# Performance work log

Measured on AMD Instinct MI355X. Metric: run time of the kernel, lower is better.

The kernel has to match this reference:

```python
import jax, jax.numpy as jnp
import numpy as np

N_CLIN = 38
N_PIX = 36
N_NODES = N_CLIN + N_PIX  # 74
FV = 128
B = 1024
HID = 512
N_OUT = 1


def _base_edges():
    # Faithful to Network.get_edges: self-edges for all nodes, then for each
    # pixel node i, bidirectional edges to every clinical node.
    ids = np.arange(N_NODES)
    parts = [np.stack([ids, ids])]
    c = np.arange(N_CLIN)
    for i in range(N_CLIN, N_NODES):
        ii = np.full(N_CLIN, i)
        parts.append(np.stack([ii, c]))
        parts.append(np.stack([c, ii]))
    return np.concatenate(parts, axis=1)  # (2, 2810)


def setup_inputs() -> dict:
    key = jax.random.key(0)
    ks = jax.random.split(key, 10)
    base = _base_edges()  # (2, E0)
    # Batched edge index: per-sample copy offset by ind*N_NODES (batch-major order,
    # matching the torch.cat loop).
    offs = np.arange(B)[None, :, None] * N_NODES  # (1, B, 1)
    edge_index = (base[:, None, :] + offs).reshape(2, -1)  # (2, B*E0)
    s = 1.0 / np.sqrt(FV)
    return {
        "clinical_embeddings": jax.random.normal(ks[0], (B, N_CLIN, FV), jnp.float32),
        "image_embeddings": jax.random.normal(ks[1], (B, N_PIX, FV), jnp.float32),
        # RMRM graph-net params (single message-passing layer, fv_dim -> fv_dim)
        "W_self": jax.random.normal(ks[2], (FV, FV), jnp.float32) * s,
        "W_msg": jax.random.normal(ks[3], (FV, FV), jnp.float32) * s,
        "b_g": jnp.zeros((FV,), jnp.float32),
        # OutputBlock MLP params: fv_dim*(n_clinical+1)=4992 -> 512 -> 1
        "W1": jax.random.normal(ks[4], (FV * (N_CLIN + 1), HID), jnp.float32) * (1.0 / np.sqrt(FV * (N_CLIN + 1))),
        "b1": jnp.zeros((HID,), jnp.float32),
        "W2": jax.random.normal(ks[5], (HID, N_OUT), jnp.float32) * (1.0 / np.sqrt(HID)),
        "b2": jnp.zeros((N_OUT,), jnp.float32),
        "edge_index": jnp.asarray(edge_index, jnp.int32),
    }


def reference(clinical_embeddings, image_embeddings, W_self, W_msg, b_g, W1, b1, W2, b2, edge_index):
    # Assemble node features: [B, n_nodes, fv] -> flat [B*n_nodes, fv]
    x = jnp.concatenate([clinical_embeddings, image_embeddings], axis=1)
    x = x.reshape(-1, FV)
    src, dst = edge_index[0], edge_index[1]
    n_total = B * N_NODES
    # Mean-aggregated message passing (RMRM layer): gather + segment-sum
    msg = jax.ops.segment_sum(x[src], dst, num_segments=n_total)  # [B*N, FV]
    deg = jax.ops.segment_sum(jnp.ones_like(src, jnp.float32), dst, num_segments=n_total)
    agg = msg / deg[:, None]
    h = jax.nn.relu(x @ W_self + agg @ W_msg + b_g)  # [B*N, FV]
    h = h.reshape(B, N_NODES, FV)
    graph_fvs_c = h[:, :N_CLIN]          # [B, 38, FV]
    graph_fvs_i = h[:, N_CLIN:]          # [B, 36, FV]
    # AvgPool2d(6,6) over [B, FV, 6, 6] == mean over the 36 pixel nodes
    gap = graph_fvs_i.mean(axis=1)       # [B, FV]
    combined = jnp.concatenate([graph_fvs_c, gap[:, None, :]], axis=1).reshape(B, -1)
    # OutputBlock MLP
    out = jax.nn.relu(combined @ W1 + b1) @ W2 + b2  # [B, 1]
    return out
```

## Files before the change

### kernel.cpp

```cpp
#include <hip/hip_runtime.h>

#define FV 128
#define NCLIN 38
#define NPIX 36
#define NTOT 74
#define BATCH 1024
#define HID 512
#define COMB 4992
#define XPAD 136

typedef __attribute__((ext_vector_type(4))) float f32x4;
typedef __attribute__((ext_vector_type(8))) short s16x8;

#define WS_WCT  0
#define WS_WIT  8192
#define WS_WMT  16384
#define WS_COMB 24576
#define WS_W1T  2580480

__device__ __forceinline__ unsigned short bf16_rne(float f) {
    union { float f; unsigned int u; } v; v.f = f;
    unsigned int u = v.u;
    u += 0x7fffu + ((u >> 16) & 1u);
    return (unsigned short)(u >> 16);
}
__device__ __forceinline__ float bf2f(unsigned short h) {
    union { unsigned int u; float f; } v; v.u = ((unsigned int)h) << 16;
    return v.f;
}

__global__ __launch_bounds__(256) void k_prep(
    const float* __restrict__ wself, const float* __restrict__ wmsg,
    const float* __restrict__ b2, float* __restrict__ ws,
    float* __restrict__ out)
{
    const int t = threadIdx.x;
    if (blockIdx.x == 8) {
        const float v = b2[0];
#pragma unroll
        for (int j = 0; j < 4; ++j) out[t + j * 256] = v;
        return;
    }
    unsigned short* WcT = (unsigned short*)(ws + WS_WCT);
    unsigned short* WiT = (unsigned short*)(ws + WS_WIT);
    unsigned short* WmT = (unsigned short*)(ws + WS_WMT);
    const int r  = blockIdx.x * 16 + (t >> 4);
    const int f0 = (t & 15) * 8;
#pragma unroll
    for (int j = 0; j < 8; ++j) {
        const int f = f0 + j;
        const int idx = r * 128 + f;
        const float wm = wmsg[idx];
        const float s  = wself[idx];
        WcT[f * 128 + r] = bf16_rne(s + wm * (1.0f / 37.0f));
        WiT[f * 128 + r] = bf16_rne(s + wm * (1.0f / 39.0f));
        WmT[f * 128 + r] = bf16_rne(wm);
    }
}

union __align__(16) SmemMain {
    float tile[64][65];
    struct {
        unsigned short xl[NTOT * XPAD];
        unsigned short sab[2 * 128];
        float tcv[128];
        float tiv[128];
    } b;
};

__global__ __launch_bounds__(256) void k_main(
    const float* __restrict__ clin, const float* __restrict__ img,
    const float* __restrict__ bg, const float* __restrict__ W1,
    float* __restrict__ ws)
{
    const int blk = blockIdx.x;
    const int t   = threadIdx.x;
    __shared__ SmemMain sm;

    if (blk >= BATCH) {
        const int u  = blk - BATCH;
        unsigned short* W1T = (unsigned short*)(ws + WS_W1T);
        const int k0 = (u >> 3) * 64;
        const int n0 = (u & 7) * 64;
        const int r16 = t >> 4;
        const int c4  = (t & 15) * 4;
#pragma unroll
        for (int p = 0; p < 4; ++p) {
            const int r = p * 16 + r16;
            const float4 v = *(const float4*)&W1[(size_t)(k0 + r) * HID + n0 + c4];
            sm.tile[r][c4 + 0] = v.x; sm.tile[r][c4 + 1] = v.y;
            sm.tile[r][c4 + 2] = v.z; sm.tile[r][c4 + 3] = v.w;
        }
        __syncthreads();
        const int j  = t >> 2;
        const int i0 = (t & 3) * 16;
        unsigned short tmp[16];
#pragma unroll
        for (int s = 0; s < 16; ++s) tmp[s] = bf16_rne(sm.tile[i0 + s][j]);
        unsigned short* dst = &W1T[(size_t)(n0 + j) * COMB + k0 + i0];
        *(uint4*)&dst[0] = *(uint4*)&tmp[0];
        *(uint4*)&dst[8] = *(uint4*)&tmp[8];
        return;
    }

    const unsigned short* WcT = (const unsigned short*)(ws + WS_WCT);
    const unsigned short* WiT = (const unsigned short*)(ws + WS_WIT);
    const unsigned short* WmT = (const unsigned short*)(ws + WS_WMT);
    const int wave = t >> 6;
    const int lane = t & 63;
    const int l16  = lane & 15;
    const int q    = lane >> 4;
    const int n0   = wave * 32 + l16;
    const int b    = blk;

    const float* xc = clin + (size_t)b * NCLIN * FV;
    const float* xi = img  + (size_t)b * NPIX * FV;
    for (int i = t; i < NCLIN * 32; i += 256) {
        const int row = i >> 5, c4 = (i & 31) * 4;
        const float4 v = *(const float4*)&xc[row * 128 + c4];
        ushort4 u;
        u.x = bf16_rne(v.x); u.y = bf16_rne(v.y);
        u.z = bf16_rne(v.z); u.w = bf16_rne(v.w);
        *(ushort4*)&sm.b.xl[row * XPAD + c4] = u;
    }
    for (int i = t; i < NPIX * 32; i += 256) {
        const int row = i >> 5, c4 = (i & 31) * 4;
        const float4 v = *(const float4*)&xi[row * 128 + c4];
        ushort4 u;
        u.x = bf16_rne(v.x); u.y = bf16_rne(v.y);
        u.z = bf16_rne(v.z); u.w = bf16_rne(v.w);
        *(ushort4*)&sm.b.xl[(NCLIN + row) * XPAD + c4] = u;
    }
    __syncthreads();

    const int f = t & 127;
    if (t < 128) {
        float s = 0.f;
#pragma unroll
        for (int n = 0; n < NCLIN; ++n) s += bf2f(sm.b.xl[n * XPAD + f]);
        sm.b.sab[128 + f] = bf16_rne(s * (1.0f / 39.0f));
    } else {
        float s = 0.f;
#pragma unroll
        for (int n = 0; n < NPIX; ++n) s += bf2f(sm.b.xl[(NCLIN + n) * XPAD + f]);
        sm.b.sab[f] = bf16_rne(s * (1.0f / 37.0f));
    }
    __syncthreads();

    {
        const int am = (l16 < 2) ? l16 : 0;
        f32x4 ta = {}, tb = {};
#pragma unroll
        for (int kk = 0; kk < 4; ++kk) {
            const int ko = kk * 32 + q * 8;
            const s16x8 av  = *(const s16x8*)&sm.b.sab[am * 128 + ko];
            const s16x8 bv0 = *(const s16x8*)&WmT[(n0)      * 128 + ko];
            const s16x8 bv1 = *(const s16x8*)&WmT[(n0 + 16) * 128 + ko];
            ta = __builtin_amdgcn_mfma_f32_16x16x32_bf16(av, bv0, ta, 0, 0, 0);
            tb = __builtin_amdgcn_mfma_f32_16x16x32_bf16(av, bv1, tb, 0, 0, 0);
        }
        if (q == 0) {
            const int c0 = wave * 32 + l16;
            const int c1 = c0 + 16;
            const float bg0 = bg[c0], bg1 = bg[c1];
            sm.b.tcv[c0] = ta[0] + bg0;  sm.b.tiv[c0] = ta[1] + bg0;
            sm.b.tcv[c1] = tb[0] + bg1;  sm.b.tiv[c1] = tb[1] + bg1;
        }
    }
    __syncthreads();

    unsigned short* combined =
        (unsigned short*)(ws + WS_COMB) + (size_t)b * COMB;

#pragma unroll
    for (int phase = 0; phase < 2; ++phase) {
        const int NN   = phase ? NPIX : NCLIN;
        const int xoff = phase ? NCLIN : 0;
        const unsigned short* WT = phase ? WiT : WcT;
        const float* tvv = phase ? sm.b.tiv : sm.b.tcv;

        const int r0 = xoff + ((l16      < NN) ? l16      : (NN - 1));
        const int r1 = xoff + ((16 + l16 < NN) ? 16 + l16 : (NN - 1));
        const int r2 = xoff + ((32 + l16 < NN) ? 32 + l16 : (NN - 1));

        f32x4 acc[3][2] = {};
#pragma unroll
        for (int kk = 0; kk < 4; ++kk) {
            const int ko = kk * 32 + q * 8;
            const s16x8 a0 = *(const s16x8*)&sm.b.xl[r0 * XPAD + ko];
            const s16x8 a1 = *(const s16x8*)&sm.b.xl[r1 * XPAD + ko];
            const s16x8 a2 = *(const s16x8*)&sm.b.xl[r2 * XPAD + ko];
            const s16x8 b0 = *(const s16x8*)&WT[(n0)      * 128 + ko];
            const s16x8 b1v = *(const s16x8*)&WT[(n0 + 16) * 128 + ko];
            acc[0][0] = __builtin_amdgcn_mfma_f32_16x16x32_bf16(a0, b0,  acc[0][0], 0, 0, 0);
            acc[0][1] = __builtin_amdgcn_mfma_f32_16x16x32_bf16(a0, b1v, acc[0][1], 0, 0, 0);
            acc[1][0] = __builtin_amdgcn_mfma_f32_16x16x32_bf16(a1, b0,  acc[1][0], 0, 0, 0);
            acc[1][1] = __builtin_amdgcn_mfma_f32_16x16x32_bf16(a1, b1v, acc[1][1], 0, 0, 0);
            acc[2][0] = __builtin_amdgcn_mfma_f32_16x16x32_bf16(a2, b0,  acc[2][0], 0, 0, 0);
            acc[2][1] = __builtin_amdgcn_mfma_f32_16x16x32_bf16(a2, b1v, acc[2][1], 0, 0, 0);
        }

        const float t0 = tvv[wave * 32 + l16];
        const float t1 = tvv[wave * 32 + 16 + l16];

        if (phase == 0) {
#pragma unroll
            for (int rt = 0; rt < 3; ++rt) {
#pragma unroll
                for (int r = 0; r < 4; ++r) {
                    const int node = rt * 16 + q * 4 + r;
                    if (node < NCLIN) {
                        combined[node * 128 + wave * 32 + l16] =
                            bf16_rne(fmaxf(acc[rt][0][r] + t0, 0.f));
                        combined[node * 128 + wave * 32 + 16 + l16] =
                            bf16_rne(fmaxf(acc[rt][1][r] + t1, 0.f));
                    }
                }
            }
        } else {
            float g0 = 0.f, g1 = 0.f;
#pragma unroll
            for (int rt = 0; rt < 3; ++rt) {
#pragma unroll
                for (int r = 0; r < 4; ++r) {
                    const int node = rt * 16 + q * 4 + r;
                    if (node < NPIX) {
                        g0 += fmaxf(acc[rt][0][r] + t0, 0.f);
                        g1 += fmaxf(acc[rt][1][r] + t1, 0.f);
                    }
                }
            }
            g0 += __shfl_xor(g0, 16); g0 += __shfl_xor(g0, 32);
            g1 += __shfl_xor(g1, 16); g1 += __shfl_xor(g1, 32);
            if (q == 0) {
                combined[NCLIN * 128 + wave * 32 + l16] =
                    bf16_rne(g0 * (1.0f / 36.0f));
                combined[NCLIN * 128 + wave * 32 + 16 + l16] =
                    bf16_rne(g1 * (1.0f / 36.0f));
            }
        }
    }
}

__global__ __launch_bounds__(256) void k_gemm_out(
    const float* __restrict__ b1, const float* __restrict__ W2,
    float* __restrict__ ws, float* __restrict__ out)
{
    const unsigned short* Abase = (const unsigned short*)(ws + WS_COMB);
    const unsigned short* Bbase = (const unsigned short*)(ws + WS_W1T);
    const int m0 = (blockIdx.x & 15) * 64;
    const int n0 = (blockIdx.x >> 4) * 64;

    __shared__ __align__(16) unsigned short As[2][64 * 64];
    __shared__ __align__(16) unsigned short Bs[2][64 * 64];

    const int t    = threadIdx.x;
    const int wave = t >> 6;
    const int lane = t & 63;
    const int wm   = (wave & 1) * 32;
    const int wn   = (wave >> 1) * 32;
    const int l16  = lane & 15;
    const int q    = lane >> 4;

    const int srow = t >> 2;
    const int c0   = (t & 3) * 2;
    const unsigned short* gA = Abase + (size_t)(m0 + srow) * COMB + c0 * 8;
    const unsigned short* gB = Bbase + (size_t)(n0 + srow) * COMB + c0 * 8;
    const int sw0 = srow * 64 + ((c0     + srow) & 7) * 8;
    const int sw1 = srow * 64 + ((c0 + 1 + srow) & 7) * 8;

    int aoff[2][2], boff[2][2];
#pragma unroll
    for (int i = 0; i < 2; ++i) {
#pragma unroll
        for (int kk = 0; kk < 2; ++kk) {
            const int rot = (kk * 4 + q + l16) & 7;
            aoff[i][kk] = (wm + 16 * i + l16) * 64 + rot * 8;
            boff[i][kk] = (wn + 16 * i + l16) * 64 + rot * 8;
        }
    }

    f32x4 acc[2][2] = {};

    *(uint4*)&As[0][sw0] = *(const uint4*)(gA);
    *(uint4*)&As[0][sw1] = *(const uint4*)(gA + 8);
    *(uint4*)&Bs[0][sw0] = *(const uint4*)(gB);
    *(uint4*)&Bs[0][sw1] = *(const uint4*)(gB + 8);

    int cur = 0;
    for (int it = 0; it < 78; ++it) {
        __syncthreads();
        if (it + 1 < 78) {
            const int kk  = (it + 1) * 64;
            const int nxt = cur ^ 1;
            *(uint4*)&As[nxt][sw0] = *(const uint4*)(gA + kk);
            *(uint4*)&As[nxt][sw1] = *(const uint4*)(gA + kk + 8);
            *(uint4*)&Bs[nxt][sw0] = *(const uint4*)(gB + kk);
            *(uint4*)&Bs[nxt][sw1] = *(const uint4*)(gB + kk + 8);
        }

#pragma unroll
        for (int kk = 0; kk < 2; ++kk) {
            const s16x8 a0 = *(const s16x8*)&As[cur][aoff[0][kk]];
            const s16x8 a1 = *(const s16x8*)&As[cur][aoff[1][kk]];
            const s16x8 b0 = *(const s16x8*)&Bs[cur][boff[0][kk]];
            const s16x8 b1v = *(const s16x8*)&Bs[cur][boff[1][kk]];
            acc[0][0] = __builtin_amdgcn_mfma_f32_16x16x32_bf16(a0, b0,  acc[0][0], 0, 0, 0);
            acc[0][1] = __builtin_amdgcn_mfma_f32_16x16x32_bf16(a0, b1v, acc[0][1], 0, 0, 0);
            acc[1][0] = __builtin_amdgcn_mfma_f32_16x16x32_bf16(a1, b0,  acc[1][0], 0, 0, 0);
            acc[1][1] = __builtin_amdgcn_mfma_f32_16x16x32_bf16(a1, b1v, acc[1][1], 0, 0, 0);
        }
        cur ^= 1;
    }

    const int colA = n0 + wn + l16;
    const int colB = colA + 16;
    const float b1a = b1[colA], b1b = b1[colB];
    const float w2a = W2[colA], w2b = W2[colB];

#pragma unroll
    for (int i = 0; i < 2; ++i) {
#pragma unroll
        for (int r = 0; r < 4; ++r) {
            const int mr = m0 + wm + 16 * i + q * 4 + r;
            float v = fmaxf(acc[i][0][r] + b1a, 0.f) * w2a
                    + fmaxf(acc[i][1][r] + b1b, 0.f) * w2b;
            v += __shfl_xor(v, 1);
            v += __shfl_xor(v, 2);
            v += __shfl_xor(v, 4);
            v += __shfl_xor(v, 8);
            if (l16 == 0) atomicAdd(&out[mr], v);
        }
    }
}

extern "C" void kernel_launch(void* const* d_in, const int* in_sizes, int n_in,
                              void* d_out, int out_size, void* d_ws, size_t ws_size,
                              hipStream_t stream) {
    const float* clin  = (const float*)d_in[0];
    const float* img   = (const float*)d_in[1];
    const float* wself = (const float*)d_in[2];
    const float* wmsg  = (const float*)d_in[3];
    const float* bg    = (const float*)d_in[4];
    const float* W1    = (const float*)d_in[5];
    const float* b1    = (const float*)d_in[6];
    const float* W2    = (const float*)d_in[7];
    const float* b2    = (const float*)d_in[8];
    float* ws  = (float*)d_ws;
    float* out = (float*)d_out;

    k_prep<<<dim3(9), 256, 0, stream>>>(wself, wmsg, b2, ws, out);
    k_main<<<dim3(BATCH + 624), 256, 0, stream>>>(clin, img, bg, W1, ws);
    k_gemm_out<<<dim3(128), 256, 0, stream>>>(b1, W2, ws, out);
}
```

Before: 175.4 us.

## Split-K the output GEMM into partial buffers with a separate reduction epilogue

The 1024x512x4992 output GEMM is split along K into 8 slices, with 64x128 tiles on a 16x4x8 grid (512 blocks instead of 128). Each slice writes fp32 partial sums to workspace. A new k_out kernel sums the partials, applies bias, ReLU and the W2 dot product, and writes the output directly, so the atomics and the b2 pre-initialisation are no longer needed. Global loads are now register-prefetched two stages ahead to overlap with MFMA. The cost is about 16 MB of extra partial-sum traffic and one more kernel launch.

```diff
diff --git a/kernel.cpp b/kernel.cpp
--- a/kernel.cpp
+++ b/kernel.cpp
@@ -17,6 +17,8 @@
 #define WS_WMT  16384
 #define WS_COMB 24576
 #define WS_W1T  2580480
+#define WS_Z    3858432
+#define ZSTRIDE (BATCH * HID)
 
 __device__ __forceinline__ unsigned short bf16_rne(float f) {
     union { float f; unsigned int u; } v; v.f = f;
@@ -31,16 +33,9 @@
 
 __global__ __launch_bounds__(256) void k_prep(
     const float* __restrict__ wself, const float* __restrict__ wmsg,
-    const float* __restrict__ b2, float* __restrict__ ws,
-    float* __restrict__ out)
+    float* __restrict__ ws)
 {
     const int t = threadIdx.x;
-    if (blockIdx.x == 8) {
-        const float v = b2[0];
-#pragma unroll
-        for (int j = 0; j < 4; ++j) out[t + j * 256] = v;
-        return;
-    }
     unsigned short* WcT = (unsigned short*)(ws + WS_WCT);
     unsigned short* WiT = (unsigned short*)(ws + WS_WIT);
     unsigned short* WmT = (unsigned short*)(ws + WS_WMT);
@@ -242,61 +237,87 @@
     }
 }
 
-__global__ __launch_bounds__(256) void k_gemm_out(
-    const float* __restrict__ b1, const float* __restrict__ W2,
-    float* __restrict__ ws, float* __restrict__ out)
+__global__ __launch_bounds__(256) void k_gemm_mfma(float* __restrict__ ws)
 {
     const unsigned short* Abase = (const unsigned short*)(ws + WS_COMB);
     const unsigned short* Bbase = (const unsigned short*)(ws + WS_W1T);
-    const int m0 = (blockIdx.x & 15) * 64;
-    const int n0 = (blockIdx.x >> 4) * 64;
+    const int m0    = blockIdx.x * 64;
+    const int n0    = blockIdx.y * 128;
+    const int ks    = blockIdx.z;
+    const int kbase = (ks < 6) ? 640 * ks : 3840 + 576 * (ks - 6);
+    const int kit   = (ks < 6) ? 10 : 9;
+    float* Z = ws + WS_Z + (size_t)ks * ZSTRIDE;
 
     __shared__ __align__(16) unsigned short As[2][64 * 64];
-    __shared__ __align__(16) unsigned short Bs[2][64 * 64];
+    __shared__ __align__(16) unsigned short Bs[2][128 * 64];
 
     const int t    = threadIdx.x;
     const int wave = t >> 6;
     const int lane = t & 63;
     const int wm   = (wave & 1) * 32;
-    const int wn   = (wave >> 1) * 32;
+    const int wn   = (wave >> 1) * 64;
     const int l16  = lane & 15;
     const int q    = lane >> 4;
 
-    const int srow = t >> 2;
-    const int c0   = (t & 3) * 2;
-    const unsigned short* gA = Abase + (size_t)(m0 + srow) * COMB + c0 * 8;
-    const unsigned short* gB = Bbase + (size_t)(n0 + srow) * COMB + c0 * 8;
-    const int sw0 = srow * 64 + ((c0     + srow) & 7) * 8;
-    const int sw1 = srow * 64 + ((c0 + 1 + srow) & 7) * 8;
-
-    int aoff[2][2], boff[2][2];
-#pragma unroll
-    for (int i = 0; i < 2; ++i) {
-#pragma unroll
-        for (int kk = 0; kk < 2; ++kk) {
-            const int rot = (kk * 4 + q + l16) & 7;
-            aoff[i][kk] = (wm + 16 * i + l16) * 64 + rot * 8;
-            boff[i][kk] = (wn + 16 * i + l16) * 64 + rot * 8;
-        }
-    }
-
-    f32x4 acc[2][2] = {};
-
-    *(uint4*)&As[0][sw0] = *(const uint4*)(gA);
-    *(uint4*)&As[0][sw1] = *(const uint4*)(gA + 8);
-    *(uint4*)&Bs[0][sw0] = *(const uint4*)(gB);
-    *(uint4*)&Bs[0][sw1] = *(const uint4*)(gB + 8);
+    const int arow = t >> 2;
+    const int ac0  = (t & 3) * 2;
+    const int brow = t >> 1;
+    const int bc0  = (t & 1) * 4;
+    const unsigned short* gA = Abase + (size_t)(m0 + arow) * COMB + kbase + ac0 * 8;
+    const unsigned short* gB = Bbase + (size_t)(n0 + brow) * COMB + kbase + bc0 * 8;
+
+    const int awo0 = arow * 64 + ((ac0     + arow) & 7) * 8;
+    const int awo1 = arow * 64 + ((ac0 + 1 + arow) & 7) * 8;
+    int bwo[4];
+#pragma unroll
+    for (int j = 0; j < 4; ++j)
+        bwo[j] = brow * 64 + ((bc0 + j + brow) & 7) * 8;
+
+    int aoff[2][2], boff[4][2];
+#pragma unroll
+    for (int kk = 0; kk < 2; ++kk) {
+#pragma unroll
+        for (int i = 0; i < 2; ++i) {
+            const int Ra = wm + 16 * i + l16;
+            aoff[i][kk] = Ra * 64 + ((kk * 4 + q + Ra) & 7) * 8;
+        }
+#pragma unroll
+        for (int j = 0; j < 4; ++j) {
+            const int Rb = wn + 16 * j + l16;
+            boff[j][kk] = Rb * 64 + ((kk * 4 + q + Rb) & 7) * 8;
+        }
+    }
+
+    f32x4 acc[2][4] = {};
+
+    uint4 pA0, pA1, pB0, pB1, pB2, pB3;
+
+    pA0 = *(const uint4*)(gA);      pA1 = *(const uint4*)(gA + 8);
+    pB0 = *(const uint4*)(gB);      pB1 = *(const uint4*)(gB + 8);
+    pB2 = *(const uint4*)(gB + 16); pB3 = *(const uint4*)(gB + 24);
+    *(uint4*)&As[0][awo0]   = pA0;  *(uint4*)&As[0][awo1]   = pA1;
+    *(uint4*)&Bs[0][bwo[0]] = pB0;  *(uint4*)&Bs[0][bwo[1]] = pB1;
+    *(uint4*)&Bs[0][bwo[2]] = pB2;  *(uint4*)&Bs[0][bwo[3]] = pB3;
+    if (kit > 1) {
+        pA0 = *(const uint4*)(gA + 64);      pA1 = *(const uint4*)(gA + 72);
+        pB0 = *(const uint4*)(gB + 64);      pB1 = *(const uint4*)(gB + 72);
+        pB2 = *(const uint4*)(gB + 80);      pB3 = *(const uint4*)(gB + 88);
+    }
 
     int cur = 0;
-    for (int it = 0; it < 78; ++it) {
+    for (int it = 0; it < kit; ++it) {
         __syncthreads();
-        if (it + 1 < 78) {
-            const int kk  = (it + 1) * 64;
-            const int nxt = cur ^ 1;
-            *(uint4*)&As[nxt][sw0] = *(const uint4*)(gA + kk);
-            *(uint4*)&As[nxt][sw1] = *(const uint4*)(gA + kk + 8);
-            *(uint4*)&Bs[nxt][sw0] = *(const uint4*)(gB + kk);
-            *(uint4*)&Bs[nxt][sw1] = *(const uint4*)(gB + kk + 8);
+        const int nxt = cur ^ 1;
+        if (it + 1 < kit) {
+            *(uint4*)&As[nxt][awo0]   = pA0;  *(uint4*)&As[nxt][awo1]   = pA1;
+            *(uint4*)&Bs[nxt][bwo[0]] = pB0;  *(uint4*)&Bs[nxt][bwo[1]] = pB1;
+            *(uint4*)&Bs[nxt][bwo[2]] = pB2;  *(uint4*)&Bs[nxt][bwo[3]] = pB3;
+        }
+        if (it + 2 < kit) {
+            const int kk = (it + 2) * 64;
+            pA0 = *(const uint4*)(gA + kk);      pA1 = *(const uint4*)(gA + kk + 8);
+            pB0 = *(const uint4*)(gB + kk);      pB1 = *(const uint4*)(gB + kk + 8);
+            pB2 = *(const uint4*)(gB + kk + 16); pB3 = *(const uint4*)(gB + kk + 24);
         }
 
 #pragma unroll
@@ -304,34 +325,56 @@
             const s16x8 a0 = *(const s16x8*)&As[cur][aoff[0][kk]];
             const s16x8 a1 = *(const s16x8*)&As[cur][aoff[1][kk]];
             const s16x8 b0 = *(const s16x8*)&Bs[cur][boff[0][kk]];
-            const s16x8 b1v = *(const s16x8*)&Bs[cur][boff[1][kk]];
-            acc[0][0] = __builtin_amdgcn_mfma_f32_16x16x32_bf16(a0, b0,  acc[0][0], 0, 0, 0);
-            acc[0][1] = __builtin_amdgcn_mfma_f32_16x16x32_bf16(a0, b1v, acc[0][1], 0, 0, 0);
-            acc[1][0] = __builtin_amdgcn_mfma_f32_16x16x32_bf16(a1, b0,  acc[1][0], 0, 0, 0);
-            acc[1][1] = __builtin_amdgcn_mfma_f32_16x16x32_bf16(a1, b1v, acc[1][1], 0, 0, 0);
+            const s16x8 b1 = *(const s16x8*)&Bs[cur][boff[1][kk]];
+            const s16x8 b2 = *(const s16x8*)&Bs[cur][boff[2][kk]];
+            const s16x8 b3 = *(const s16x8*)&Bs[cur][boff[3][kk]];
+            acc[0][0] = __builtin_amdgcn_mfma_f32_16x16x32_bf16(a0, b0, acc[0][0], 0, 0, 0);
+            acc[0][1] = __builtin_amdgcn_mfma_f32_16x16x32_bf16(a0, b1, acc[0][1], 0, 0, 0);
+            acc[0][2] = __builtin_amdgcn_mfma_f32_16x16x32_bf16(a0, b2, acc[0][2], 0, 0, 0);
+            acc[0][3] = __builtin_amdgcn_mfma_f32_16x16x32_bf16(a0, b3, acc[0][3], 0, 0, 0);
+            acc[1][0] = __builtin_amdgcn_mfma_f32_16x16x32_bf16(a1, b0, acc[1][0], 0, 0, 0);
+            acc[1][1] = __builtin_amdgcn_mfma_f32_16x16x32_bf16(a1, b1, acc[1][1], 0, 0, 0);
+            acc[1][2] = __builtin_amdgcn_mfma_f32_16x16x32_bf16(a1, b2, acc[1][2], 0, 0, 0);
+            acc[1][3] = __builtin_amdgcn_mfma_f32_16x16x32_bf16(a1, b3, acc[1][3], 0, 0, 0);
         }
         cur ^= 1;
     }
-
-    const int colA = n0 + wn + l16;
-    const int colB = colA + 16;
-    const float b1a = b1[colA], b1b = b1[colB];
-    const float w2a = W2[colA], w2b = W2[colB];
 
 #pragma unroll
     for (int i = 0; i < 2; ++i) {
 #pragma unroll
         for (int r = 0; r < 4; ++r) {
             const int mr = m0 + wm + 16 * i + q * 4 + r;
-            float v = fmaxf(acc[i][0][r] + b1a, 0.f) * w2a
-                    + fmaxf(acc[i][1][r] + b1b, 0.f) * w2b;
-            v += __shfl_xor(v, 1);
-            v += __shfl_xor(v, 2);
-            v += __shfl_xor(v, 4);
-            v += __shfl_xor(v, 8);
-            if (l16 == 0) atomicAdd(&out[mr], v);
-        }
-    }
+            float* zr = Z + (size_t)mr * HID + n0 + wn + l16;
+#pragma unroll
+            for (int j = 0; j < 4; ++j) {
+                zr[16 * j] = acc[i][j][r];
+            }
+        }
+    }
+}
+
+__global__ __launch_bounds__(256) void k_out(
+    const float* __restrict__ b1, const float* __restrict__ W2,
+    const float* __restrict__ b2, const float* __restrict__ ws,
+    float* __restrict__ out)
+{
+    const int b = blockIdx.x * 4 + (threadIdx.x >> 6);
+    const int l = threadIdx.x & 63;
+    const float* z = ws + WS_Z + (size_t)b * HID;
+    float s = 0.f;
+#pragma unroll
+    for (int j = 0; j < 8; ++j) {
+        const int h = l + j * 64;
+        float acc = b1[h];
+#pragma unroll
+        for (int p = 0; p < 8; ++p) acc += z[(size_t)p * ZSTRIDE + h];
+        acc = fmaxf(acc, 0.f);
+        s += acc * W2[h];
+    }
+#pragma unroll
+    for (int off = 32; off > 0; off >>= 1) s += __shfl_down(s, off);
+    if (l == 0) out[b] = s + b2[0];
 }
 
 extern "C" void kernel_launch(void* const* d_in, const int* in_sizes, int n_in,
@@ -349,7 +392,8 @@
     float* ws  = (float*)d_ws;
     float* out = (float*)d_out;
 
-    k_prep<<<dim3(9), 256, 0, stream>>>(wself, wmsg, b2, ws, out);
+    k_prep<<<dim3(8), 256, 0, stream>>>(wself, wmsg, ws);
     k_main<<<dim3(BATCH + 624), 256, 0, stream>>>(clin, img, bg, W1, ws);
-    k_gemm_out<<<dim3(128), 256, 0, stream>>>(b1, W2, ws, out);
-}
+    k_gemm_mfma<<<dim3(16, 4, 8), 256, 0, stream>>>(ws);
+    k_out<<<dim3(BATCH / 4), 256, 0, stream>>>(b1, W2, b2, ws, out);
+}
```

New measurement: 144.4 us. 1.21x faster.
